# Performance work log

Measured on AMD Instinct MI355X. Metric: run time of the kernel, lower is better.

The kernel has to match this reference:

```python
import jax, jax.numpy as jnp
import numpy as np

N = 50000      # nodes
E = 500000     # edges
D_IN = 64      # node_in_dim
K = 4          # edge_in_dim
H = 64         # node_hidden_dim
C = 40         # num_class
L = 2          # num_layers


def setup_inputs() -> dict:
    key = jax.random.key(0)
    ks = jax.random.split(key, 10)
    node_features = jax.random.normal(ks[0], (N, D_IN), jnp.float32)
    edge_features = jax.random.normal(ks[1], (L, E, K), jnp.float32)
    src = jax.random.randint(ks[2], (E,), 0, N)
    dst = jax.random.randint(ks[3], (E,), 0, N)
    W0 = jax.random.normal(ks[4], (K * D_IN, H), jnp.float32) * 0.05
    b0 = jnp.zeros((H,), jnp.float32)
    W1 = jax.random.normal(ks[5], (K * H, H), jnp.float32) * 0.05
    b1 = jnp.zeros((H,), jnp.float32)
    Wfc = jax.random.normal(ks[6], (H, C), jnp.float32) * 0.05
    bfc = jnp.zeros((C,), jnp.float32)
    return dict(node_features=node_features, edge_features=edge_features,
                src=src, dst=dst, W0=W0, b0=b0, W1=W1, b1=b1, Wfc=Wfc, bfc=bfc)


def reference(node_features, edge_features, src, dst, W0, b0, W1, b1, Wfc, bfc):
    h = node_features  # [N, d]
    ones = jnp.ones((E,), jnp.float32)
    cnt = jnp.maximum(jax.ops.segment_sum(ones, dst, num_segments=N), 1.0)  # in-degree
    for i, (W, b) in enumerate([(W0, b0), (W1, b1)]):
        e = edge_features[i]          # [E, K]
        hs = h[src]                   # [E, d] edge gather of src node features
        d = hs.shape[1]
        # message: relu(Linear(flatten(e[:,:,None] * h[:,None,:])))
        # flatten order is (K, d), so reshape W -> [K, d, H] and contract directly
        Wr = W.reshape(K, d, H)
        m = jax.nn.relu(jnp.einsum('ek,ed,kdh->eh', e, hs, Wr) + b)  # [E, H]
        s = jax.ops.segment_sum(m, dst, num_segments=N)              # scatter-sum
        h = jax.nn.relu(s / cnt[:, None])                            # mailbox mean + relu
    return h @ Wfc + bfc  # [N, C]
```

## Files before the change

kernel.cpp:

```cpp
#include <hip/hip_runtime.h>
#include <hip/hip_fp16.h>

#define N_NODES 50000
#define N_EDGES 500000
#define DIM 64
#define KDIM 4
#define HID 64
#define NCLS 40
#define NBLK ((N_NODES + 255) / 256)

__device__ inline unsigned pack2(float a, float b) {
    __half2 h = __floats2half2_rn(a, b);
    return *(unsigned*)&h;
}
__device__ inline float2 unpack2(unsigned u) {
    __half2 h = *(__half2*)&u;
    return __half22float2(h);
}

__global__ void hist_k(const int* __restrict__ dst, int* __restrict__ cnt) {
    int e = blockIdx.x * 256 + threadIdx.x;
    if (e < N_EDGES) atomicAdd(&cnt[dst[e]], 1);
}

__global__ __launch_bounds__(256) void scan_k(const int* __restrict__ cnt,
                                              int* __restrict__ start,
                                              int* __restrict__ cursor,
                                              volatile int* __restrict__ bflag,
                                              volatile int* __restrict__ bval) {
    __shared__ int ls[256];
    __shared__ int sbase;
    __shared__ int ok_all;
    int b = blockIdx.x, t = threadIdx.x;
    int n = b * 256 + t;
    int v = (n < N_NODES) ? cnt[n] : 0;
    ls[t] = v;
    __syncthreads();
#pragma unroll
    for (int off = 1; off < 256; off <<= 1) {
        int u = (t >= off) ? ls[t - off] : 0;
        __syncthreads();
        ls[t] += u;
        __syncthreads();
    }
    int incl = ls[t];
    int total = ls[255];
    __syncthreads();

    if (t == 0) {
        bval[b] = total;
        __threadfence();
        bflag[b] = 1;
    }

    if (b > 0) {
        for (;;) {
            int f = (t < b) ? bflag[t] : 1;
            if (t == 0) ok_all = 1;
            __syncthreads();
            if (!f) ok_all = 0;
            __syncthreads();
            if (ok_all) break;
        }
        __threadfence();
        int pv = (t < b) ? bval[t] : 0;
        ls[t] = pv;
        __syncthreads();
#pragma unroll
        for (int off = 128; off > 0; off >>= 1) {
            if (t < off) ls[t] += ls[t + off];
            __syncthreads();
        }
        if (t == 0) sbase = ls[0];
        __syncthreads();
    } else {
        if (t == 0) sbase = 0;
        __syncthreads();
    }

    int excl = sbase + incl - v;
    if (n < N_NODES) { start[n] = excl; cursor[n] = excl; }
    if (n == 0) start[N_NODES] = N_EDGES;
}

__global__ void scatter_k(const int* __restrict__ src, const int* __restrict__ dst,
                          const float* __restrict__ ef, int* __restrict__ cursor,
                          uint4* __restrict__ rec) {
    int e = blockIdx.x * 256 + threadIdx.x;
    if (e < N_EDGES) {
        int d = dst[e];
        int pos = atomicAdd(&cursor[d], 1);
        int sn = src[e];
        float4 f0 = ((const float4*)ef)[e];
        float4 f1 = ((const float4*)ef)[N_EDGES + e];
        rec[2 * pos]     = make_uint4((unsigned)sn, pack2(f0.x, f0.y), pack2(f0.z, f0.w), 0u);
        rec[2 * pos + 1] = make_uint4((unsigned)sn, pack2(f1.x, f1.y), pack2(f1.z, f1.w), 0u);
    }
}

__global__ __launch_bounds__(256) void transform_k(const float* __restrict__ hin,
                                                   const float* __restrict__ W,
                                                   unsigned* __restrict__ y) {
    __shared__ float sW[KDIM * 64 * 64];
    __shared__ float sh[32 * 65];
    int t = threadIdx.x;

    const float4* W4 = (const float4*)W;
    float4* sW4 = (float4*)sW;
#pragma unroll
    for (int i = 0; i < 16; ++i) sW4[t + 256 * i] = W4[t + 256 * i];

    int n0 = blockIdx.x * 32;
#pragma unroll
    for (int i = 0; i < 2; ++i) {
        int idx = t + 256 * i;
        int nl = idx >> 4;
        int dg = idx & 15;
        int n = n0 + nl;
        float4 v = make_float4(0.f, 0.f, 0.f, 0.f);
        if (n < N_NODES) v = ((const float4*)hin)[(size_t)n * 16 + dg];
        sh[nl * 65 + dg * 4 + 0] = v.x;
        sh[nl * 65 + dg * 4 + 1] = v.y;
        sh[nl * 65 + dg * 4 + 2] = v.z;
        sh[nl * 65 + dg * 4 + 3] = v.w;
    }
    __syncthreads();

    int nl = t & 15;
    int cg = t >> 4;
    int k = cg >> 2;
    int hc0 = (cg & 3) * 16;

    float acc0[16], acc1[16];
#pragma unroll
    for (int j = 0; j < 16; ++j) { acc0[j] = 0.f; acc1[j] = 0.f; }

    for (int d = 0; d < 64; ++d) {
        float a0 = sh[nl * 65 + d];
        float a1 = sh[(nl + 16) * 65 + d];
        const float* wr = &sW[k * 4096 + d * 64 + hc0];
#pragma unroll
        for (int j = 0; j < 16; ++j) {
            float w = wr[j];
            acc0[j] = fmaf(a0, w, acc0[j]);
            acc1[j] = fmaf(a1, w, acc1[j]);
        }
    }

    int n_a = n0 + nl, n_b = n0 + nl + 16;
    int cbase = k * 64 + hc0;
    if (n_a < N_NODES) {
        uint4* o = (uint4*)(y + ((size_t)n_a * 256 + cbase) / 2);
        o[0] = make_uint4(pack2(acc0[0], acc0[1]), pack2(acc0[2], acc0[3]),
                          pack2(acc0[4], acc0[5]), pack2(acc0[6], acc0[7]));
        o[1] = make_uint4(pack2(acc0[8], acc0[9]), pack2(acc0[10], acc0[11]),
                          pack2(acc0[12], acc0[13]), pack2(acc0[14], acc0[15]));
    }
    if (n_b < N_NODES) {
        uint4* o = (uint4*)(y + ((size_t)n_b * 256 + cbase) / 2);
        o[0] = make_uint4(pack2(acc1[0], acc1[1]), pack2(acc1[2], acc1[3]),
                          pack2(acc1[4], acc1[5]), pack2(acc1[6], acc1[7]));
        o[1] = make_uint4(pack2(acc1[8], acc1[9]), pack2(acc1[10], acc1[11]),
                          pack2(acc1[12], acc1[13]), pack2(acc1[14], acc1[15]));
    }
}

__device__ inline void edge_step(const uint4 r, const unsigned* __restrict__ y,
                                 int lane, const float4 bias, float4& acc) {
    int sn = (int)r.x;
    float2 e01 = unpack2(r.y);
    float2 e23 = unpack2(r.z);
    const uint2* yb = (const uint2*)(y + (size_t)sn * 128);
    uint2 q0 = yb[lane];
    uint2 q1 = yb[16 + lane];
    uint2 q2 = yb[32 + lane];
    uint2 q3 = yb[48 + lane];

    float2 a0 = unpack2(q0.x), a1 = unpack2(q0.y);
    float2 b0 = unpack2(q1.x), b1 = unpack2(q1.y);
    float2 c0 = unpack2(q2.x), c1 = unpack2(q2.y);
    float2 d0 = unpack2(q3.x), d1 = unpack2(q3.y);

    float4 z = bias;
    z.x = fmaf(e01.x, a0.x, z.x); z.y = fmaf(e01.x, a0.y, z.y);
    z.z = fmaf(e01.x, a1.x, z.z); z.w = fmaf(e01.x, a1.y, z.w);
    z.x = fmaf(e01.y, b0.x, z.x); z.y = fmaf(e01.y, b0.y, z.y);
    z.z = fmaf(e01.y, b1.x, z.z); z.w = fmaf(e01.y, b1.y, z.w);
    z.x = fmaf(e23.x, c0.x, z.x); z.y = fmaf(e23.x, c0.y, z.y);
    z.z = fmaf(e23.x, c1.x, z.z); z.w = fmaf(e23.x, c1.y, z.w);
    z.x = fmaf(e23.y, d0.x, z.x); z.y = fmaf(e23.y, d0.y, z.y);
    z.z = fmaf(e23.y, d1.x, z.z); z.w = fmaf(e23.y, d1.y, z.w);

    acc.x += fmaxf(z.x, 0.f);
    acc.y += fmaxf(z.y, 0.f);
    acc.z += fmaxf(z.z, 0.f);
    acc.w += fmaxf(z.w, 0.f);
}

__device__ inline float4 agg_core(const uint4* __restrict__ rec2,
                                  const int* __restrict__ start,
                                  const int* __restrict__ cnt,
                                  const unsigned* __restrict__ y,
                                  const float* __restrict__ b,
                                  int g, int lane) {
    int s0 = start[g];
    int deg = cnt[g];
    int s1 = s0 + deg;

    float4 bias = ((const float4*)b)[lane];
    float4 acc = make_float4(0.f, 0.f, 0.f, 0.f);

    int i = s0;
    for (; i + 2 <= s1; i += 2) {
        uint4 r0 = rec2[2 * i];
        uint4 r1 = rec2[2 * (i + 1)];
        edge_step(r0, y, lane, bias, acc);
        edge_step(r1, y, lane, bias, acc);
    }
    if (i < s1) {
        uint4 r0 = rec2[2 * i];
        edge_step(r0, y, lane, bias, acc);
    }

    float inv = 1.0f / (float)(deg > 1 ? deg : 1);
    float4 r;
    r.x = fmaxf(acc.x * inv, 0.f);
    r.y = fmaxf(acc.y * inv, 0.f);
    r.z = fmaxf(acc.z * inv, 0.f);
    r.w = fmaxf(acc.w * inv, 0.f);
    return r;
}

__global__ __launch_bounds__(256) void agg_k(const uint4* __restrict__ rec2,
                                             const int* __restrict__ start,
                                             const int* __restrict__ cnt,
                                             const unsigned* __restrict__ y,
                                             const float* __restrict__ b,
                                             float* __restrict__ hout) {
    int t = blockIdx.x * 256 + threadIdx.x;
    int g = t >> 4;
    int lane = t & 15;
    float4 r = agg_core(rec2, start, cnt, y, b, g, lane);
    ((float4*)hout)[(size_t)g * 16 + lane] = r;
}

__global__ __launch_bounds__(256) void agg_fc_k(const uint4* __restrict__ rec2,
                                                const int* __restrict__ start,
                                                const int* __restrict__ cnt,
                                                const unsigned* __restrict__ y,
                                                const float* __restrict__ b,
                                                const float* __restrict__ Wfc,
                                                const float* __restrict__ bfc,
                                                float* __restrict__ out) {
    __shared__ float sh_h[16 * 65];
    __shared__ float sWfc[64 * NCLS];
    __shared__ float sbfc[NCLS];
    int t = threadIdx.x;

    for (int i = t; i < 64 * NCLS; i += 256) sWfc[i] = Wfc[i];
    if (t < NCLS) sbfc[t] = bfc[t];

    int nl = t >> 4;
    int lane = t & 15;
    int g = blockIdx.x * 16 + nl;

    float4 r = agg_core(rec2, start, cnt, y, b, g, lane);
    sh_h[nl * 65 + lane * 4 + 0] = r.x;
    sh_h[nl * 65 + lane * 4 + 1] = r.y;
    sh_h[nl * 65 + lane * 4 + 2] = r.z;
    sh_h[nl * 65 + lane * 4 + 3] = r.w;
    __syncthreads();

    for (int item = t; item < 16 * NCLS; item += 256) {
        int rn = item / NCLS;
        int c = item - rn * NCLS;
        float acc = sbfc[c];
        const float* hr = &sh_h[rn * 65];
#pragma unroll
        for (int j = 0; j < 64; ++j) acc = fmaf(hr[j], sWfc[j * NCLS + c], acc);
        out[(size_t)(blockIdx.x * 16 + rn) * NCLS + c] = acc;
    }
}

extern "C" void kernel_launch(void* const* d_in, const int* in_sizes, int n_in,
                              void* d_out, int out_size, void* d_ws, size_t ws_size,
                              hipStream_t stream) {
    const float* nf  = (const float*)d_in[0];
    const float* ef  = (const float*)d_in[1];
    const int*   src = (const int*)d_in[2];
    const int*   dst = (const int*)d_in[3];
    const float* W0  = (const float*)d_in[4];
    const float* b0  = (const float*)d_in[5];
    const float* W1  = (const float*)d_in[6];
    const float* b1  = (const float*)d_in[7];
    const float* Wfc = (const float*)d_in[8];
    const float* bfc = (const float*)d_in[9];
    float* out = (float*)d_out;

    char* ws = (char*)d_ws;
    size_t off = 0;
    auto alloc = [&](size_t bytes) -> void* {
        void* p = ws + off;
        off = (off + bytes + 255) & ~(size_t)255;
        return p;
    };
    int*      zbuf   = (int*)     alloc((size_t)(50176 + 512) * 4);
    int*      cnt    = zbuf;
    int*      bflag  = zbuf + 50176;
    int*      bval   = zbuf + 50176 + 256;
    int*      start  = (int*)     alloc((size_t)(N_NODES + 1) * 4);
    int*      cursor = (int*)     alloc((size_t)N_NODES * 4);
    uint4*    rec    = (uint4*)   alloc((size_t)N_EDGES * 32);
    unsigned* y      = (unsigned*)alloc((size_t)N_NODES * 256 * 2);
    float*    hbuf   = (float*)   alloc((size_t)N_NODES * 64 * 4);

    hipMemsetAsync(zbuf, 0, (size_t)(50176 + 512) * 4, stream);

    hist_k<<<(N_EDGES + 255) / 256, 256, 0, stream>>>(dst, cnt);
    scan_k<<<NBLK, 256, 0, stream>>>(cnt, start, cursor, bflag, bval);
    scatter_k<<<(N_EDGES + 255) / 256, 256, 0, stream>>>(src, dst, ef, cursor, rec);

    int tgrid = (N_NODES + 31) / 32;
    int agrid = N_NODES / 16;

    transform_k<<<tgrid, 256, 0, stream>>>(nf, W0, y);
    agg_k<<<agrid, 256, 0, stream>>>(rec, start, cnt, y, b0, hbuf);

    transform_k<<<tgrid, 256, 0, stream>>>(hbuf, W1, y);
    agg_fc_k<<<agrid, 256, 0, stream>>>(rec + 1, start, cnt, y, b1, Wfc, bfc, out);
}
```

Measured before the change: 308.6 us.

## Split transform over K pairs, batch gather loads in aggregation, transpose FC weights

The transform kernel now gives each block 64 nodes and only two of the four K slices, using a 2D grid. This halves the weight tile per block in shared memory and doubles the node reuse of each loaded weight. The aggregation loop issues the gathered loads for four edges before any compute, giving more memory-level parallelism at the cost of extra registers. The FC weights are stored transposed and padded in shared memory so the inner loop reads them contiguously.

```diff
diff --git a/kernel.cpp b/kernel.cpp
--- a/kernel.cpp
+++ b/kernel.cpp
@@ -101,18 +101,19 @@
 __global__ __launch_bounds__(256) void transform_k(const float* __restrict__ hin,
                                                    const float* __restrict__ W,
                                                    unsigned* __restrict__ y) {
-    __shared__ float sW[KDIM * 64 * 64];
-    __shared__ float sh[32 * 65];
+    __shared__ float sW[2 * 64 * 64];
+    __shared__ float sh[64 * 65];
     int t = threadIdx.x;
-
-    const float4* W4 = (const float4*)W;
+    int kpair = blockIdx.y;
+
+    const float4* W4 = (const float4*)(W + (size_t)kpair * 2 * 4096);
     float4* sW4 = (float4*)sW;
 #pragma unroll
-    for (int i = 0; i < 16; ++i) sW4[t + 256 * i] = W4[t + 256 * i];
-
-    int n0 = blockIdx.x * 32;
-#pragma unroll
-    for (int i = 0; i < 2; ++i) {
+    for (int i = 0; i < 8; ++i) sW4[t + 256 * i] = W4[t + 256 * i];
+
+    int n0 = blockIdx.x * 64;
+#pragma unroll
+    for (int i = 0; i < 4; ++i) {
         int idx = t + 256 * i;
         int nl = idx >> 4;
         int dg = idx & 15;
@@ -126,9 +127,9 @@
     }
     __syncthreads();
 
-    int nl = t & 15;
-    int cg = t >> 4;
-    int k = cg >> 2;
+    int nl = t & 31;
+    int cg = t >> 5;
+    int k_local = cg >> 2;
     int hc0 = (cg & 3) * 16;
 
     float acc0[16], acc1[16];
@@ -137,8 +138,8 @@
 
     for (int d = 0; d < 64; ++d) {
         float a0 = sh[nl * 65 + d];
-        float a1 = sh[(nl + 16) * 65 + d];
-        const float* wr = &sW[k * 4096 + d * 64 + hc0];
+        float a1 = sh[(nl + 32) * 65 + d];
+        const float* wr = &sW[k_local * 4096 + d * 64 + hc0];
 #pragma unroll
         for (int j = 0; j < 16; ++j) {
             float w = wr[j];
@@ -147,8 +148,8 @@
         }
     }
 
-    int n_a = n0 + nl, n_b = n0 + nl + 16;
-    int cbase = k * 64 + hc0;
+    int n_a = n0 + nl, n_b = n0 + nl + 32;
+    int cbase = (kpair * 2 + k_local) * 64 + hc0;
     if (n_a < N_NODES) {
         uint4* o = (uint4*)(y + ((size_t)n_a * 256 + cbase) / 2);
         o[0] = make_uint4(pack2(acc0[0], acc0[1]), pack2(acc0[2], acc0[3]),
@@ -165,17 +166,20 @@
     }
 }
 
-__device__ inline void edge_step(const uint4 r, const unsigned* __restrict__ y,
-                                 int lane, const float4 bias, float4& acc) {
+__device__ inline void load_edge(const uint4 r, const unsigned* __restrict__ y,
+                                 int lane, uint2& q0, uint2& q1, uint2& q2, uint2& q3) {
     int sn = (int)r.x;
+    const uint2* yb = (const uint2*)(y + (size_t)sn * 128);
+    q0 = yb[lane];
+    q1 = yb[16 + lane];
+    q2 = yb[32 + lane];
+    q3 = yb[48 + lane];
+}
+
+__device__ inline void compute_edge(const uint4 r, uint2 q0, uint2 q1, uint2 q2, uint2 q3,
+                                    const float4 bias, float4& acc) {
     float2 e01 = unpack2(r.y);
     float2 e23 = unpack2(r.z);
-    const uint2* yb = (const uint2*)(y + (size_t)sn * 128);
-    uint2 q0 = yb[lane];
-    uint2 q1 = yb[16 + lane];
-    uint2 q2 = yb[32 + lane];
-    uint2 q3 = yb[48 + lane];
-
     float2 a0 = unpack2(q0.x), a1 = unpack2(q0.y);
     float2 b0 = unpack2(q1.x), b1 = unpack2(q1.y);
     float2 c0 = unpack2(q2.x), c1 = unpack2(q2.y);
@@ -211,15 +215,36 @@
     float4 acc = make_float4(0.f, 0.f, 0.f, 0.f);
 
     int i = s0;
-    for (; i + 2 <= s1; i += 2) {
-        uint4 r0 = rec2[2 * i];
-        uint4 r1 = rec2[2 * (i + 1)];
-        edge_step(r0, y, lane, bias, acc);
-        edge_step(r1, y, lane, bias, acc);
+    for (; i + 4 <= s1; i += 4) {
+        uint4 r0 = rec2[2 * i + 0];
+        uint4 r1 = rec2[2 * i + 2];
+        uint4 r2 = rec2[2 * i + 4];
+        uint4 r3 = rec2[2 * i + 6];
+        uint2 a0, a1, a2, a3, b0, b1, b2, b3, c0, c1, c2, c3, d0, d1, d2, d3;
+        load_edge(r0, y, lane, a0, a1, a2, a3);
+        load_edge(r1, y, lane, b0, b1, b2, b3);
+        load_edge(r2, y, lane, c0, c1, c2, c3);
+        load_edge(r3, y, lane, d0, d1, d2, d3);
+        compute_edge(r0, a0, a1, a2, a3, bias, acc);
+        compute_edge(r1, b0, b1, b2, b3, bias, acc);
+        compute_edge(r2, c0, c1, c2, c3, bias, acc);
+        compute_edge(r3, d0, d1, d2, d3, bias, acc);
+    }
+    if (i + 2 <= s1) {
+        uint4 r0 = rec2[2 * i + 0];
+        uint4 r1 = rec2[2 * i + 2];
+        uint2 a0, a1, a2, a3, b0, b1, b2, b3;
+        load_edge(r0, y, lane, a0, a1, a2, a3);
+        load_edge(r1, y, lane, b0, b1, b2, b3);
+        compute_edge(r0, a0, a1, a2, a3, bias, acc);
+        compute_edge(r1, b0, b1, b2, b3, bias, acc);
+        i += 2;
     }
     if (i < s1) {
         uint4 r0 = rec2[2 * i];
-        edge_step(r0, y, lane, bias, acc);
+        uint2 a0, a1, a2, a3;
+        load_edge(r0, y, lane, a0, a1, a2, a3);
+        compute_edge(r0, a0, a1, a2, a3, bias, acc);
     }
 
     float inv = 1.0f / (float)(deg > 1 ? deg : 1);
@@ -253,11 +278,15 @@
                                                 const float* __restrict__ bfc,
                                                 float* __restrict__ out) {
     __shared__ float sh_h[16 * 65];
-    __shared__ float sWfc[64 * NCLS];
+    __shared__ float sWfcT[NCLS * 65];
     __shared__ float sbfc[NCLS];
     int t = threadIdx.x;
 
-    for (int i = t; i < 64 * NCLS; i += 256) sWfc[i] = Wfc[i];
+    for (int i = t; i < 64 * NCLS; i += 256) {
+        int j = i / NCLS;
+        int c = i - j * NCLS;
+        sWfcT[c * 65 + j] = Wfc[i];
+    }
     if (t < NCLS) sbfc[t] = bfc[t];
 
     int nl = t >> 4;
@@ -276,8 +305,9 @@
         int c = item - rn * NCLS;
         float acc = sbfc[c];
         const float* hr = &sh_h[rn * 65];
-#pragma unroll
-        for (int j = 0; j < 64; ++j) acc = fmaf(hr[j], sWfc[j * NCLS + c], acc);
+        const float* wc = &sWfcT[c * 65];
+#pragma unroll
+        for (int j = 0; j < 64; ++j) acc = fmaf(hr[j], wc[j], acc);
         out[(size_t)(blockIdx.x * 16 + rn) * NCLS + c] = acc;
     }
 }
@@ -320,7 +350,7 @@
     scan_k<<<NBLK, 256, 0, stream>>>(cnt, start, cursor, bflag, bval);
     scatter_k<<<(N_EDGES + 255) / 256, 256, 0, stream>>>(src, dst, ef, cursor, rec);
 
-    int tgrid = (N_NODES + 31) / 32;
+    dim3 tgrid((N_NODES + 63) / 64, 2);
     int agrid = N_NODES / 16;
 
     transform_k<<<tgrid, 256, 0, stream>>>(nf, W0, y);
```

Result: faster. 300.1 us (-2.8%).
